# Kernel tuning notes

Measured on AMD Instinct MI355X. Metric: run time of the kernel, lower is better.

The kernel has to match this reference:

```python
import jax, jax.numpy as jnp
import numpy as np

ALPHA, GAMMA = 0.25, 2.0
EPS_CLS, EPS_DICE = 1e-8, 1e-5


def box_cxcywh_to_xyxy(b):
    cx, cy, w, h = b[..., 0], b[..., 1], b[..., 2], b[..., 3]
    return jnp.stack([cx - 0.5 * w, cy - 0.5 * h, cx + 0.5 * w, cy + 0.5 * h], axis=-1)


def generalized_box_iou(b1, b2):
    # b1: [N,4], b2: [T,4] in xyxy -> [N,T]
    area1 = (b1[:, 2] - b1[:, 0]) * (b1[:, 3] - b1[:, 1])
    area2 = (b2[:, 2] - b2[:, 0]) * (b2[:, 3] - b2[:, 1])
    lt = jnp.maximum(b1[:, None, :2], b2[None, :, :2])
    rb = jnp.minimum(b1[:, None, 2:], b2[None, :, 2:])
    wh = jnp.clip(rb - lt, 0.0)
    inter = wh[..., 0] * wh[..., 1]
    union = area1[:, None] + area2[None, :] - inter
    iou = inter / union
    lt_e = jnp.minimum(b1[:, None, :2], b2[None, :, :2])
    rb_e = jnp.maximum(b1[:, None, 2:], b2[None, :, 2:])
    wh_e = jnp.clip(rb_e - lt_e, 0.0)
    area_e = wh_e[..., 0] * wh_e[..., 1]
    return iou - (area_e - union) / area_e


def masks_to_boxes(masks):
    # DETR util: masks [N,H,W] (any float; nonzero treated as 'on') -> xyxy [N,4]
    n, h, w = masks.shape
    x = jnp.arange(w, dtype=masks.dtype)
    y = jnp.arange(h, dtype=masks.dtype)
    nz = masks != 0
    x_mask = masks * x[None, None, :]
    x_max = x_mask.reshape(n, -1).max(-1)
    x_min = jnp.where(nz, x_mask, 1e8).reshape(n, -1).min(-1)
    y_mask = masks * y[None, :, None]
    y_max = y_mask.reshape(n, -1).max(-1)
    y_min = jnp.where(nz, y_mask, 1e8).reshape(n, -1).min(-1)
    return jnp.stack([x_min, y_min, x_max, y_max], axis=1)


def setup_inputs() -> dict:
    key = jax.random.key(0)
    k1, k2, k3, k4, k5, k6 = jax.random.split(key, 6)
    return {
        'pred_logits': jax.random.normal(k1, (2, 300, 91), dtype=jnp.float32),
        'pred_boxes': jax.random.uniform(k2, (2, 300, 4), dtype=jnp.float32),
        'pred_masks': jax.random.normal(k3, (2, 300, 256, 256), dtype=jnp.float32),
        'tgt_boxes': jax.random.uniform(k4, (60, 4), dtype=jnp.float32),
        'tgt_ids': jax.random.randint(k5, (60,), 0, 91, dtype=jnp.int64) if jax.config.jax_enable_x64 else jax.random.randint(k5, (60,), 0, 91).astype(jnp.int32),
        'tgt_masks': jax.random.randint(k6, (60, 256, 256), 0, 2, dtype=jnp.int32),
    }


def reference(pred_logits, pred_boxes, pred_masks, tgt_boxes, tgt_ids, tgt_masks):
    bs, Q, C = pred_logits.shape
    N = bs * Q
    tgt_masks_f = tgt_masks.astype(pred_masks.dtype)

    # --- focal classification cost ---
    out_prob = jax.nn.sigmoid(pred_logits.reshape(N, C))
    neg_cc = (1 - ALPHA) * out_prob ** GAMMA * -jnp.log(1 - out_prob + EPS_CLS)
    pos_cc = ALPHA * (1 - out_prob) ** GAMMA * -jnp.log(out_prob + EPS_CLS)
    cost_class = pos_cc[:, tgt_ids] - neg_cc[:, tgt_ids]  # [N,T]

    # --- L1 box cost (cdist p=1) ---
    out_bbox = pred_boxes.reshape(N, 4)
    cost_bbox = jnp.abs(out_bbox[:, None, :] - tgt_boxes[None, :, :]).sum(-1)

    # --- GIoU box cost ---
    cost_giou = -generalized_box_iou(box_cxcywh_to_xyxy(out_bbox),
                                     box_cxcywh_to_xyxy(tgt_boxes))

    # --- GIoU on mask-derived boxes (faithful to original, incl. cxcywh conversion) ---
    out_mask = pred_masks.reshape(N, pred_masks.shape[2], pred_masks.shape[3])
    cost_giou_m2b = -generalized_box_iou(
        box_cxcywh_to_xyxy(masks_to_boxes(out_mask)),
        box_cxcywh_to_xyxy(masks_to_boxes(tgt_masks_f)))

    # --- pairwise dice cost: batched matmul instead of the O(N*T) python loop ---
    HW = out_mask.shape[1] * out_mask.shape[2]
    p = jax.nn.sigmoid(out_mask).reshape(N, HW)      # [N,HW]
    t = tgt_masks_f.reshape(tgt_masks_f.shape[0], HW)  # [T,HW] binary
    inter = p @ t.T                                   # [N,T]
    union = p.sum(1)[:, None] + t.sum(1)[None, :]
    cost_mask_dice = 1.0 - (2 * inter + EPS_DICE) / (union + EPS_DICE)

    # --- pairwise focal cost; exact closed form for binary targets:
    # focal(i,j) = mean_px[ t*pos_px + (1-t)*neg_px ]
    pos_px = ALPHA * (1 - p) ** GAMMA * -jnp.log(p)
    neg_px = (1 - ALPHA) * p ** GAMMA * -jnp.log(1 - p)
    cost_mask_focal = (pos_px @ t.T + neg_px.sum(1)[:, None] - neg_px @ t.T) / HW

    Cmat = (cost_bbox + cost_class + cost_giou +
            cost_giou_m2b + cost_mask_dice + cost_mask_focal)
    return Cmat.reshape(bs, Q, -1)
```

## Files before the change

kernel.cpp:

```cpp
#include <hip/hip_runtime.h>
#include <math.h>

#define HW    65536
#define TNUM  60
#define NPRED 600
#define NCLS  91
#define PS    16
#define NTIL  38

typedef float f32x4 __attribute__((ext_vector_type(4)));
typedef short s16x8 __attribute__((ext_vector_type(8)));

__global__ void hm_tgt_stats(const int* __restrict__ tm, float* __restrict__ tstat) {
    int j = blockIdx.x >> 3, chunk = blockIdx.x & 7;
    int tid = threadIdx.x;
    const int* row = tm + (size_t)j * HW + chunk * 8192;
    float cnt = 0.f, xmax = -INFINITY, ymax = -INFINITY, xmin = INFINITY, ymin = INFINITY;
    for (int i = tid; i < 8192; i += 256) {
        int pix = chunk * 8192 + i;
        float t = (float)row[i];
        float xf = (float)(pix & 255), yf = (float)(pix >> 8);
        float xm = t * xf, ym = t * yf;
        cnt += t;
        xmax = fmaxf(xmax, xm); ymax = fmaxf(ymax, ym);
        bool nz = (t != 0.f);
        xmin = fminf(xmin, nz ? xm : 1e8f);
        ymin = fminf(ymin, nz ? ym : 1e8f);
    }
#pragma unroll
    for (int o = 1; o < 64; o <<= 1) {
        cnt += __shfl_xor(cnt, o);
        xmax = fmaxf(xmax, __shfl_xor(xmax, o));
        ymax = fmaxf(ymax, __shfl_xor(ymax, o));
        xmin = fminf(xmin, __shfl_xor(xmin, o));
        ymin = fminf(ymin, __shfl_xor(ymin, o));
    }
    __shared__ float s[5][4];
    int w = tid >> 6;
    if ((tid & 63) == 0) { s[0][w]=cnt; s[1][w]=xmin; s[2][w]=ymin; s[3][w]=xmax; s[4][w]=ymax; }
    __syncthreads();
    if (tid == 0) {
        float* o = tstat + (size_t)(j * 8 + chunk) * 5;
        o[0] = s[0][0]+s[0][1]+s[0][2]+s[0][3];
        o[1] = fminf(fminf(s[1][0],s[1][1]),fminf(s[1][2],s[1][3]));
        o[2] = fminf(fminf(s[2][0],s[2][1]),fminf(s[2][2],s[2][3]));
        o[3] = fmaxf(fmaxf(s[3][0],s[3][1]),fmaxf(s[3][2],s[3][3]));
        o[4] = fmaxf(fmaxf(s[4][0],s[4][1]),fmaxf(s[4][2],s[4][3]));
    }
}

__global__ void hm_build_tpack(const int* __restrict__ tm, unsigned short* __restrict__ tp) {
    int bid = blockIdx.x;
    int j = bid >> 8, chunk = bid & 255;
    int pix = chunk * 256 + threadIdx.x;
    unsigned short v = 0;
    if (j < TNUM) v = (tm[(size_t)j * HW + pix] != 0) ? (unsigned short)0x3F80 : (unsigned short)0;
    size_t idx = ((size_t)(pix >> 5) * 64 + j) * 32 + (size_t)((pix >> 3) & 3) * 8 + (pix & 7);
    tp[idx] = v;
}

__device__ inline void pix_proc(float x, int e, float xfb, float yf,
                                __bf16* P, __bf16* F,
                                float& sp, float& sn,
                                float& xM, float& yM, float& xm, float& ym) {
    float ex = __expf(x);
    float opex = 1.f + ex;
    float p = __fdividef(ex, opex);
    float spx = __logf(opex);
    float spmx = spx - x;
    float om = 1.f - p;
    float pos = 0.25f * om * om * spmx;
    float neg = 0.75f * p * p * spx;
    sp += p; sn += neg;
    float xf = xfb + (float)e;
    float xmsk = x * xf, ymsk = x * yf;
    xM = fmaxf(xM, xmsk); yM = fmaxf(yM, ymsk);
    bool nz = (x != 0.f);
    xm = fminf(xm, nz ? xmsk : 1e8f);
    ym = fminf(ym, nz ? ymsk : 1e8f);
    P[e] = (__bf16)p;
    F[e] = (__bf16)(pos - neg);
}

__launch_bounds__(256, 2)
__global__ void hm_heavy(const float* __restrict__ pm, const unsigned short* __restrict__ tp,
                         float* __restrict__ dots, float* __restrict__ stats) {
    int b = blockIdx.x;
    int ntile = b >> 4, ps = b & 15;
    int tid = threadIdx.x, w = tid >> 6, l = tid & 63, g = l >> 4, c = l & 15;
    int n0 = ntile * 16;
    int row = min(n0 + c, NPRED - 1);
    const float* A = pm + (size_t)row * HW;
    const s16x8* tpv = (const s16x8*)tp;
    int pb = ps * 4096 + w * 1024;

    f32x4 acc[4][2];
#pragma unroll
    for (int nt = 0; nt < 4; ++nt)
#pragma unroll
        for (int m = 0; m < 2; ++m) acc[nt][m] = (f32x4)0.f;

    float sp = 0.f, sn = 0.f;
    float xM = -INFINITY, yM = -INFINITY, xm = INFINITY, ym = INFINITY;

#pragma unroll 2
    for (int step = 0; step < 32; ++step) {
        int k0 = pb + step * 32;
        int kk = k0 + g * 8;
        float4 aa = *(const float4*)(A + kk);
        float4 ab = *(const float4*)(A + kk + 4);
        float yf = (float)(kk >> 8);
        float xfb = (float)(kk & 255);

        union { __bf16 h[8]; s16x8 v; } P, F;
        float x[8] = {aa.x, aa.y, aa.z, aa.w, ab.x, ab.y, ab.z, ab.w};
#pragma unroll
        for (int e = 0; e < 8; ++e)
            pix_proc(x[e], e, xfb, yf, P.h, F.h, sp, sn, xM, yM, xm, ym);

        int bbase = (k0 >> 5) * 256 + c * 4 + g;
#pragma unroll
        for (int nt = 0; nt < 4; ++nt) {
            s16x8 bf = tpv[bbase + nt * 64];
            acc[nt][0] = __builtin_amdgcn_mfma_f32_16x16x32_bf16(P.v, bf, acc[nt][0], 0, 0, 0);
            acc[nt][1] = __builtin_amdgcn_mfma_f32_16x16x32_bf16(F.v, bf, acc[nt][1], 0, 0, 0);
        }
    }

#pragma unroll
    for (int o = 16; o <= 32; o <<= 1) {
        sp += __shfl_xor(sp, o); sn += __shfl_xor(sn, o);
        xM = fmaxf(xM, __shfl_xor(xM, o)); yM = fmaxf(yM, __shfl_xor(yM, o));
        xm = fminf(xm, __shfl_xor(xm, o)); ym = fminf(ym, __shfl_xor(ym, o));
    }

    __shared__ float ldsD[4][32][64];
    __shared__ float ldsS[4][16][6];
#pragma unroll
    for (int nt = 0; nt < 4; ++nt)
#pragma unroll
        for (int m = 0; m < 2; ++m)
#pragma unroll
            for (int r = 0; r < 4; ++r)
                ldsD[w][(nt * 2 + m) * 4 + r][l] = acc[nt][m][r];
    if (l < 16) {
        ldsS[w][l][0] = sp; ldsS[w][l][1] = sn;
        ldsS[w][l][2] = xM; ldsS[w][l][3] = yM;
        ldsS[w][l][4] = xm; ldsS[w][l][5] = ym;
    }
    __syncthreads();

    for (int idx = tid; idx < 2048; idx += 256) {
        int mat = idx >> 10, rl = (idx >> 6) & 15, col = idx & 63;
        int gg = rl >> 2, rg = rl & 3;
        int nt = col >> 4, cc = col & 15;
        int lane = gg * 16 + cc;
        int off = (nt * 2 + mat) * 4 + rg;
        float s = ldsD[0][off][lane] + ldsD[1][off][lane] + ldsD[2][off][lane] + ldsD[3][off][lane];
        dots[(size_t)b * 2048 + idx] = s;
    }
    if (tid < 96) {
        int rr = tid / 6, s = tid % 6;
        float a0 = ldsS[0][rr][s], a1 = ldsS[1][rr][s], a2 = ldsS[2][rr][s], a3 = ldsS[3][rr][s];
        float r;
        if (s < 2)      r = a0 + a1 + a2 + a3;
        else if (s < 4) r = fmaxf(fmaxf(a0, a1), fmaxf(a2, a3));
        else            r = fminf(fminf(a0, a1), fminf(a2, a3));
        stats[(size_t)(b * 16 + rr) * 6 + s] = r;
    }
}

__global__ void hm_pred_reduce(const float* __restrict__ stats, float* __restrict__ pstat) {
    int n = blockIdx.x;
    int l = threadIdx.x;
    int ntile = n >> 4, r = n & 15;
    int ps = l & 15;
    const float* sb = stats + ((size_t)((ntile * PS + ps) * 16 + r)) * 6;
    float v0 = sb[0], v1 = sb[1], v2 = sb[2], v3 = sb[3], v4 = sb[4], v5 = sb[5];
#pragma unroll
    for (int o = 1; o < 16; o <<= 1) {
        v0 += __shfl_xor(v0, o); v1 += __shfl_xor(v1, o);
        v2 = fmaxf(v2, __shfl_xor(v2, o)); v3 = fmaxf(v3, __shfl_xor(v3, o));
        v4 = fminf(v4, __shfl_xor(v4, o)); v5 = fminf(v5, __shfl_xor(v5, o));
    }
    if (l == 0) {
        float* o = pstat + (size_t)n * 6;
        o[0] = v0; o[1] = v1; o[2] = v2; o[3] = v3; o[4] = v4; o[5] = v5;
    }
}

__device__ inline float giou2(float ax0, float ay0, float ax1, float ay1,
                              float bx0, float by0, float bx1, float by1) {
    float area1 = (ax1 - ax0) * (ay1 - ay0);
    float area2 = (bx1 - bx0) * (by1 - by0);
    float ltx = fmaxf(ax0, bx0), lty = fmaxf(ay0, by0);
    float rbx = fminf(ax1, bx1), rby = fminf(ay1, by1);
    float iw = fmaxf(rbx - ltx, 0.f), ih = fmaxf(rby - lty, 0.f);
    float inter = iw * ih;
    float uni = area1 + area2 - inter;
    float iou = inter / uni;
    float ex0 = fminf(ax0, bx0), ey0 = fminf(ay0, by0);
    float ex1 = fmaxf(ax1, bx1), ey1 = fmaxf(ay1, by1);
    float ew = fmaxf(ex1 - ex0, 0.f), eh = fmaxf(ey1 - ey0, 0.f);
    float ae = ew * eh;
    return iou - (ae - uni) / ae;
}

__device__ inline float giou_cxcywh(float acx, float acy, float aw, float ah,
                                    float bcx, float bcy, float bw, float bh) {
    return giou2(acx - 0.5f * aw, acy - 0.5f * ah, acx + 0.5f * aw, acy + 0.5f * ah,
                 bcx - 0.5f * bw, bcy - 0.5f * bh, bcx + 0.5f * bw, bcy + 0.5f * bh);
}

__global__ void hm_combine(const float* __restrict__ pred_logits,
                           const float* __restrict__ pred_boxes,
                           const float* __restrict__ tgt_boxes,
                           const int* __restrict__ tgt_ids,
                           const float* __restrict__ dots,
                           const float* __restrict__ pstat,
                           const float* __restrict__ tstat,
                           float* __restrict__ out) {
    int idx = blockIdx.x * blockDim.x + threadIdx.x;
    if (idx >= NPRED * TNUM) return;
    int n = idx / TNUM, j = idx % TNUM;
    int ntile = n >> 4, r = n & 15;

    const float* db = dots + (size_t)ntile * PS * 2048 + r * 64 + j;
    float dp = 0.f, df = 0.f;
#pragma unroll
    for (int ps = 0; ps < PS; ++ps) {
        dp += db[ps * 2048];
        df += db[ps * 2048 + 1024];
    }

    float tcnt = 0.f, txm = INFINITY, tym = INFINITY, txM = -INFINITY, tyM = -INFINITY;
#pragma unroll
    for (int k = 0; k < 8; ++k) {
        const float* tb = tstat + (size_t)(j * 8 + k) * 5;
        tcnt += tb[0];
        txm = fminf(txm, tb[1]); tym = fminf(tym, tb[2]);
        txM = fmaxf(txM, tb[3]); tyM = fmaxf(tyM, tb[4]);
    }

    const float* pp = pstat + (size_t)n * 6;
    float sum_p = pp[0], sum_neg = pp[1];
    float pxM = pp[2], pyM = pp[3], pxm = pp[4], pym = pp[5];

    float4 ob = ((const float4*)pred_boxes)[n];
    float4 tb4 = ((const float4*)tgt_boxes)[j];
    float cbbox = fabsf(ob.x - tb4.x) + fabsf(ob.y - tb4.y) + fabsf(ob.z - tb4.z) + fabsf(ob.w - tb4.w);

    float cgiou = -giou_cxcywh(ob.x, ob.y, ob.z, ob.w, tb4.x, tb4.y, tb4.z, tb4.w);

    int id = tgt_ids[j];
    float lg = pred_logits[(size_t)n * NCLS + id];
    float e = __expf(lg);
    float pr = __fdividef(e, 1.f + e);
    float poscc = 0.25f * (1.f - pr) * (1.f - pr) * (-__logf(pr + 1e-8f));
    float negcc = 0.75f * pr * pr * (-__logf(1.f - pr + 1e-8f));
    float cclass = poscc - negcc;

    float cm2b = -giou_cxcywh(pxm, pym, pxM, pyM, txm, tym, txM, tyM);

    float un = sum_p + tcnt;
    float cdice = 1.f - (2.f * dp + 1e-5f) / (un + 1e-5f);

    float cfocal = (df + sum_neg) * (1.0f / (float)HW);

    out[idx] = cbbox + cclass + cgiou + cm2b + cdice + cfocal;
}

extern "C" void kernel_launch(void* const* d_in, const int* in_sizes, int n_in,
                              void* d_out, int out_size, void* d_ws, size_t ws_size,
                              hipStream_t stream) {
    const float* pred_logits = (const float*)d_in[0];
    const float* pred_boxes  = (const float*)d_in[1];
    const float* pred_masks  = (const float*)d_in[2];
    const float* tgt_boxes   = (const float*)d_in[3];
    const int*   tgt_ids     = (const int*)d_in[4];
    const int*   tgt_masks   = (const int*)d_in[5];
    float* out = (float*)d_out;

    char* wsb = (char*)d_ws;
    unsigned short* tpack = (unsigned short*)wsb;
    float* dots  = (float*)(wsb + 8388608);
    float* stats = (float*)(wsb + 8388608 + 4980736);
    float* pstat = (float*)(wsb + 8388608 + 4980736 + 233472);
    float* tstat = (float*)(wsb + 8388608 + 4980736 + 233472 + 14400);

    hipLaunchKernelGGL(hm_tgt_stats, dim3(TNUM * 8), dim3(256), 0, stream, tgt_masks, tstat);
    hipLaunchKernelGGL(hm_build_tpack, dim3(64 * 256), dim3(256), 0, stream, tgt_masks, tpack);
    hipLaunchKernelGGL(hm_heavy, dim3(NTIL * PS), dim3(256), 0, stream, pred_masks, tpack, dots, stats);
    hipLaunchKernelGGL(hm_pred_reduce, dim3(NPRED), dim3(64), 0, stream, stats, pstat);
    hipLaunchKernelGGL(hm_combine, dim3((NPRED * TNUM + 255) / 256), dim3(256), 0, stream,
                       pred_logits, pred_boxes, tgt_boxes, tgt_ids, dots, pstat, tstat, out);
}
```

Baseline: 116.0 us.

## Double pixel-split blocks, swizzle block IDs across XCDs, write per-wave stats directly

Splits the pixel dimension of the heavy MFMA kernel into 32 slices instead of 16, doubling the grid and halving per-block work. Block IDs are remapped so consecutive IDs spread pixel slices across the 8 XCDs, and launch bounds now target 4 blocks per CU. Per-wave mask statistics go straight to global memory and the reduce kernel now folds 128 partials per row, dropping the LDS stats reduction. The aim is better occupancy and load balance, at the cost of more partial dot-product writes and a larger reduction in the combine stage.

```diff
diff --git a/kernel.cpp b/kernel.cpp
--- a/kernel.cpp
+++ b/kernel.cpp
@@ -5,7 +5,7 @@
 #define TNUM  60
 #define NPRED 600
 #define NCLS  91
-#define PS    16
+#define PS    32
 #define NTIL  38
 
 typedef float f32x4 __attribute__((ext_vector_type(4)));
@@ -69,8 +69,8 @@
     float spx = __logf(opex);
     float spmx = spx - x;
     float om = 1.f - p;
-    float pos = 0.25f * om * om * spmx;
-    float neg = 0.75f * p * p * spx;
+    float pos = (om * om) * (0.25f * spmx);
+    float neg = (p * p) * (0.75f * spx);
     sp += p; sn += neg;
     float xf = xfb + (float)e;
     float xmsk = x * xf, ymsk = x * yf;
@@ -82,17 +82,19 @@
     F[e] = (__bf16)(pos - neg);
 }
 
-__launch_bounds__(256, 2)
+__launch_bounds__(256, 4)
 __global__ void hm_heavy(const float* __restrict__ pm, const unsigned short* __restrict__ tp,
                          float* __restrict__ dots, float* __restrict__ stats) {
-    int b = blockIdx.x;
-    int ntile = b >> 4, ps = b & 15;
+    int id = blockIdx.x;
+    int xcd = id & 7, q = id >> 3;
+    int ntile = q % NTIL, ps = xcd + 8 * (q / NTIL);
+    int bl = ntile * PS + ps;
     int tid = threadIdx.x, w = tid >> 6, l = tid & 63, g = l >> 4, c = l & 15;
     int n0 = ntile * 16;
     int row = min(n0 + c, NPRED - 1);
     const float* A = pm + (size_t)row * HW;
     const s16x8* tpv = (const s16x8*)tp;
-    int pb = ps * 4096 + w * 1024;
+    int pb = ps * 2048 + w * 512;
 
     f32x4 acc[4][2];
 #pragma unroll
@@ -104,7 +106,7 @@
     float xM = -INFINITY, yM = -INFINITY, xm = INFINITY, ym = INFINITY;
 
 #pragma unroll 2
-    for (int step = 0; step < 32; ++step) {
+    for (int step = 0; step < 16; ++step) {
         int k0 = pb + step * 32;
         int kk = k0 + g * 8;
         float4 aa = *(const float4*)(A + kk);
@@ -133,9 +135,12 @@
         xM = fmaxf(xM, __shfl_xor(xM, o)); yM = fmaxf(yM, __shfl_xor(yM, o));
         xm = fminf(xm, __shfl_xor(xm, o)); ym = fminf(ym, __shfl_xor(ym, o));
     }
+    if (l < 16) {
+        float* so = stats + ((size_t)((bl * 4 + w) * 16 + l)) * 6;
+        so[0] = sp; so[1] = sn; so[2] = xM; so[3] = yM; so[4] = xm; so[5] = ym;
+    }
 
     __shared__ float ldsD[4][32][64];
-    __shared__ float ldsS[4][16][6];
 #pragma unroll
     for (int nt = 0; nt < 4; ++nt)
 #pragma unroll
@@ -143,11 +148,6 @@
 #pragma unroll
             for (int r = 0; r < 4; ++r)
                 ldsD[w][(nt * 2 + m) * 4 + r][l] = acc[nt][m][r];
-    if (l < 16) {
-        ldsS[w][l][0] = sp; ldsS[w][l][1] = sn;
-        ldsS[w][l][2] = xM; ldsS[w][l][3] = yM;
-        ldsS[w][l][4] = xm; ldsS[w][l][5] = ym;
-    }
     __syncthreads();
 
     for (int idx = tid; idx < 2048; idx += 256) {
@@ -157,16 +157,7 @@
         int lane = gg * 16 + cc;
         int off = (nt * 2 + mat) * 4 + rg;
         float s = ldsD[0][off][lane] + ldsD[1][off][lane] + ldsD[2][off][lane] + ldsD[3][off][lane];
-        dots[(size_t)b * 2048 + idx] = s;
-    }
-    if (tid < 96) {
-        int rr = tid / 6, s = tid % 6;
-        float a0 = ldsS[0][rr][s], a1 = ldsS[1][rr][s], a2 = ldsS[2][rr][s], a3 = ldsS[3][rr][s];
-        float r;
-        if (s < 2)      r = a0 + a1 + a2 + a3;
-        else if (s < 4) r = fmaxf(fmaxf(a0, a1), fmaxf(a2, a3));
-        else            r = fminf(fminf(a0, a1), fminf(a2, a3));
-        stats[(size_t)(b * 16 + rr) * 6 + s] = r;
+        dots[(size_t)bl * 2048 + idx] = s;
     }
 }
 
@@ -174,11 +165,16 @@
     int n = blockIdx.x;
     int l = threadIdx.x;
     int ntile = n >> 4, r = n & 15;
-    int ps = l & 15;
-    const float* sb = stats + ((size_t)((ntile * PS + ps) * 16 + r)) * 6;
-    float v0 = sb[0], v1 = sb[1], v2 = sb[2], v3 = sb[3], v4 = sb[4], v5 = sb[5];
-#pragma unroll
-    for (int o = 1; o < 16; o <<= 1) {
+    const float* s0 = stats + ((size_t)(ntile * 128 + l) * 16 + r) * 6;
+    const float* s1 = stats + ((size_t)(ntile * 128 + l + 64) * 16 + r) * 6;
+    float v0 = s0[0] + s1[0];
+    float v1 = s0[1] + s1[1];
+    float v2 = fmaxf(s0[2], s1[2]);
+    float v3 = fmaxf(s0[3], s1[3]);
+    float v4 = fminf(s0[4], s1[4]);
+    float v5 = fminf(s0[5], s1[5]);
+#pragma unroll
+    for (int o = 1; o < 64; o <<= 1) {
         v0 += __shfl_xor(v0, o); v1 += __shfl_xor(v1, o);
         v2 = fmaxf(v2, __shfl_xor(v2, o)); v3 = fmaxf(v3, __shfl_xor(v3, o));
         v4 = fminf(v4, __shfl_xor(v4, o)); v5 = fminf(v5, __shfl_xor(v5, o));
@@ -284,9 +280,9 @@
     char* wsb = (char*)d_ws;
     unsigned short* tpack = (unsigned short*)wsb;
     float* dots  = (float*)(wsb + 8388608);
-    float* stats = (float*)(wsb + 8388608 + 4980736);
-    float* pstat = (float*)(wsb + 8388608 + 4980736 + 233472);
-    float* tstat = (float*)(wsb + 8388608 + 4980736 + 233472 + 14400);
+    float* stats = (float*)(wsb + 18350080);
+    float* pstat = (float*)(wsb + 20217856);
+    float* tstat = (float*)(wsb + 20232256);
 
     hipLaunchKernelGGL(hm_tgt_stats, dim3(TNUM * 8), dim3(256), 0, stream, tgt_masks, tstat);
     hipLaunchKernelGGL(hm_build_tpack, dim3(64 * 256), dim3(256), 0, stream, tgt_masks, tpack);
```

New measurement: 94.07 us. -18.9%, faster.
